# Performance work log

Measured on AMD Instinct MI355X. Metric: run time of the kernel, lower is better.

Reference implementation:

```python
import jax, jax.numpy as jnp
import numpy as np

Y0 = 0.28209479177387814  # Y_0^0 spherical harmonic (degree-0 basis)
CUTOFF = 4.6
K_COUL = 0.529
ENERGY_STD = 1.0
HEADS = 8
N, E, C, L, MID = 32768, 524288, 16, 4, 32
KC = C // 2  # channels_div = 2 -> key/value channels


def _radial(ef, W1, b1, W2, b2, W3, b3):
    # radial profile MLP producing per-edge conv weights
    h = jax.nn.relu(ef @ W1 + b1)
    h = jax.nn.relu(h @ W2 + b2)
    return h @ W3 + b3


def _conv_msg(x_src, ef, bscale, W1, b1, W2, b2, W3, b3, c_out, c_in):
    # degree-0 tensor-field conv: per-edge weight matrix times source feats, times basis
    R = _radial(ef, W1, b1, W2, b2, W3, b3).reshape(-1, c_out, c_in)
    return jnp.einsum('eoi,ei->eo', R, x_src) * bscale[:, None]


def _forward(species, src, dst, rel_pos, emb, kv_W1, kv_b1, kv_W2, kv_b2, kv_W3, kv_b3, Wq, Wproj, fin_W1, fin_b1, fin_W2, fin_b2, fin_W3, fin_b3, Wself, mlp_W1, mlp_b1, mlp_W2, mlp_b2, mlp_W3, mlp_b3):
    n = species.shape[0]
    dist = jnp.linalg.norm(rel_pos, axis=1)
    xc = dist / CUTOFF
    in_cut = dist < CUTOFF
    x2 = jnp.minimum(jnp.where(in_cut, xc * xc, 0.0), 1.0 - 1e-6)
    scale = jnp.where(in_cut, jnp.exp(3.0 - 3.0 / (1.0 - x2)), 0.0)  # bump_fn k=3
    bscale = Y0 * scale  # basis scaled by cutoff envelope per edge
    semb = emb[species - 1]          # [N,C]
    x = semb                         # degree-0 node feats
    # edge feats: (C-1) zero radial-basis channels + distance
    ef = jnp.concatenate([jnp.zeros((dist.shape[0], C - 1), dist.dtype), dist[:, None]], axis=1)
    dh = KC // HEADS
    for l in range(kv_W1.shape[0]):
        kv = _conv_msg(x[src], ef, bscale, kv_W1[l], kv_b1[l], kv_W2[l], kv_b2[l], kv_W3[l], kv_b3[l], 2 * KC, C)
        val, key_ = kv[:, :KC], kv[:, KC:]
        q = x @ Wq[l].T              # [N,KC]
        logits = jnp.einsum('ehd,ehd->eh', key_.reshape(-1, HEADS, dh), q[dst].reshape(-1, HEADS, dh)) / np.sqrt(dh)
        mx = jax.ops.segment_max(logits, dst, num_segments=n)
        w = scale[:, None] * jnp.exp(logits - mx[dst])   # weighted edge softmax
        denom = jax.ops.segment_sum(w, dst, num_segments=n)
        attn = w / jnp.maximum(denom[dst], 1e-20)
        z = (attn[:, :, None] * val.reshape(-1, HEADS, dh)).reshape(-1, KC)
        agg = jax.ops.segment_sum(z, dst, num_segments=n)
        x = jnp.concatenate([agg, x], axis=1) @ Wproj[l].T  # project(cat(attn_out, skip))
        ef = ef + x[src]             # edge feature update via copy_u
    m = _conv_msg(x[src], ef, bscale, fin_W1, fin_b1, fin_W2, fin_b2, fin_W3, fin_b3, C, C)
    feats = jax.ops.segment_sum(m, dst, num_segments=n) + x @ Wself.T  # pooled conv + self-interaction
    cat = jnp.concatenate([semb, feats], axis=1)
    h = jax.nn.silu(cat @ mlp_W1 + mlp_b1)
    h = jax.nn.silu(h @ mlp_W2 + mlp_b2)
    learned = (h @ mlp_W3 + mlp_b3)[:, 0]
    Z = species.astype(dist.dtype)
    Zu, Zv = Z[src], Z[dst]
    raw = K_COUL * Zu * Zv / (2.0 * dist)
    au = 0.8854 * 0.529 / (Zu ** 0.23 + Zv ** 0.23)
    xx = dist / au
    screen = (0.1818 * jnp.exp(-3.2 * xx) + 0.5099 * jnp.exp(-0.9423 * xx)
              + 0.2802 * jnp.exp(-0.4028 * xx) + 0.02817 * jnp.exp(-0.2016 * xx))
    coul = jax.ops.segment_sum(raw * screen * scale, dst, num_segments=n) / ENERGY_STD
    atom_e = (learned + coul) * ENERGY_STD
    return jnp.sum(atom_e)  # SumPooling over a single graph, forces=False


def setup_inputs() -> dict:
    key = jax.random.key(0)
    ks = jax.random.split(key, 32)
    species = jax.random.randint(ks[0], (N,), 1, 90, dtype=jnp.int32)
    src = jax.random.randint(ks[1], (E,), 0, N, dtype=jnp.int32)
    dst = jax.random.randint(ks[2], (E,), 0, N, dtype=jnp.int32)
    d = jax.random.normal(ks[3], (E, 3))
    d = d / jnp.linalg.norm(d, axis=1, keepdims=True)
    r = jax.random.uniform(ks[4], (E, 1), minval=0.5, maxval=5.5)
    rel_pos = (d * r).astype(jnp.float32)
    g = lambda k, sh, fan: (jax.random.normal(k, sh) / np.sqrt(fan)).astype(jnp.float32)
    return dict(
        species=species, src=src, dst=dst, rel_pos=rel_pos,
        emb=g(ks[5], (100, C), 1),
        kv_W1=g(ks[6], (L, C, MID), C), kv_b1=jnp.zeros((L, MID), jnp.float32),
        kv_W2=g(ks[7], (L, MID, MID), MID), kv_b2=jnp.zeros((L, MID), jnp.float32),
        kv_W3=g(ks[8], (L, MID, 2 * KC * C), MID), kv_b3=jnp.zeros((L, 2 * KC * C), jnp.float32),
        Wq=g(ks[9], (L, KC, C), C),
        Wproj=g(ks[10], (L, C, KC + C), KC + C),
        fin_W1=g(ks[11], (C, MID), C), fin_b1=jnp.zeros((MID,), jnp.float32),
        fin_W2=g(ks[12], (MID, MID), MID), fin_b2=jnp.zeros((MID,), jnp.float32),
        fin_W3=g(ks[13], (MID, C * C), MID), fin_b3=jnp.zeros((C * C,), jnp.float32),
        Wself=g(ks[14], (C, C), C),
        mlp_W1=g(ks[15], (2 * C, C), 2 * C), mlp_b1=jnp.zeros((C,), jnp.float32),
        mlp_W2=g(ks[16], (C, C), C), mlp_b2=jnp.zeros((C,), jnp.float32),
        mlp_W3=g(ks[17], (C, 1), C), mlp_b3=jnp.zeros((1,), jnp.float32),
    )


def reference(species, src, dst, rel_pos, emb, kv_W1, kv_b1, kv_W2, kv_b2, kv_W3, kv_b3, Wq, Wproj, fin_W1, fin_b1, fin_W2, fin_b2, fin_W3, fin_b3, Wself, mlp_W1, mlp_b1, mlp_W2, mlp_b2, mlp_W3, mlp_b3):
    return _forward(species, src, dst, rel_pos, emb, kv_W1, kv_b1, kv_W2, kv_b2, kv_W3, kv_b3, Wq, Wproj, fin_W1, fin_b1, fin_W2, fin_b2, fin_W3, fin_b3, Wself, mlp_W1, mlp_b1, mlp_W2, mlp_b2, mlp_W3, mlp_b3)
```

## Files before the change

kernel.cpp:

```cpp
#include <hip/hip_runtime.h>

constexpr float F_Y0     = 0.28209479177387814f;
constexpr float F_CUTOFF = 4.6f;

typedef short short8 __attribute__((ext_vector_type(8)));
typedef float f32x4  __attribute__((ext_vector_type(4)));
typedef float float2v __attribute__((ext_vector_type(2)));

__device__ __forceinline__ float siluf(float v) { return v / (1.0f + __expf(-v)); }

__device__ __forceinline__ unsigned pk2(float a, float b) {
  unsigned r;
  asm("v_cvt_pk_bf16_f32 %0, %1, %2" : "=v"(r) : "v"(a), "v"(b));
  return r;
}
__device__ __forceinline__ float xbf(unsigned d, int h) {
  return __uint_as_float(h ? (d & 0xffff0000u) : (d << 16));
}
__device__ __forceinline__ float2v pkmul2(float2v a, float2v b) {
  float2v d;
  asm("v_pk_mul_f32 %0, %1, %2" : "=v"(d) : "v"(a), "v"(b));
  return d;
}

union FragU { uint4 u; short8 s; };

__device__ __forceinline__ void load16(const float* p, float* r) {
  const float4* p4 = (const float4*)p;
#pragma unroll
  for (int i = 0; i < 4; i++) {
    float4 t = p4[i];
    r[4*i] = t.x; r[4*i+1] = t.y; r[4*i+2] = t.z; r[4*i+3] = t.w;
  }
}
__device__ __forceinline__ void store16(float* p, const float* r) {
  float4* p4 = (float4*)p;
#pragma unroll
  for (int i = 0; i < 4; i++) p4[i] = make_float4(r[4*i], r[4*i+1], r[4*i+2], r[4*i+3]);
}

__device__ __forceinline__ void block_reduce_store(float v, float* part) {
  __shared__ float sred[4];
  int tid = threadIdx.x;
#pragma unroll
  for (int off = 32; off > 0; off >>= 1) v += __shfl_down(v, off, 64);
  if ((tid & 63) == 0) sred[tid >> 6] = v;
  __syncthreads();
  if (tid == 0) part[blockIdx.x] = sred[0] + sred[1] + sred[2] + sred[3];
}

__global__ __launch_bounds__(256) void k_pre(
    const int* __restrict__ species, const int* __restrict__ src, const int* __restrict__ dst,
    const float* __restrict__ rel_pos,
    float* __restrict__ dist_, float* __restrict__ scale_,
    int* __restrict__ cnt,
    float* __restrict__ coul_part, int E)
{
  int e = blockIdx.x * 256 + threadIdx.x;
  float ce = 0.0f;
  if (e < E) {
    float px = rel_pos[3*(size_t)e + 0];
    float py = rel_pos[3*(size_t)e + 1];
    float pz = rel_pos[3*(size_t)e + 2];
    float dist = sqrtf(px*px + py*py + pz*pz);
    float xc = dist * (1.0f / F_CUTOFF);
    bool in_cut = dist < F_CUTOFF;
    float x2 = in_cut ? xc * xc : 0.0f;
    x2 = fminf(x2, 1.0f - 1e-6f);
    float sc = in_cut ? __expf(3.0f - 3.0f / (1.0f - x2)) : 0.0f;
    dist_[e] = dist;
    scale_[e] = sc;
    atomicAdd(&cnt[dst[e]], 1);
    float Zu = (float)species[src[e]];
    float Zv = (float)species[dst[e]];
    float raw = 0.529f * Zu * Zv / (2.0f * dist);
    float au = 0.8854f * 0.529f / (__powf(Zu, 0.23f) + __powf(Zv, 0.23f));
    float xx = dist / au;
    float screen = 0.1818f   * __expf(-3.2f    * xx)
                 + 0.5099f   * __expf(-0.9423f * xx)
                 + 0.2802f   * __expf(-0.4028f * xx)
                 + 0.02817f  * __expf(-0.2016f * xx);
    ce = raw * screen * sc;
  }
  block_reduce_store(ce, coul_part);
}

__global__ __launch_bounds__(256) void k_scan1(
    const int* __restrict__ cnt, int* __restrict__ row_ptr, int* __restrict__ bsum)
{
  __shared__ int s[256];
  int tid = threadIdx.x;
  int n = blockIdx.x * 256 + tid;
  int v = cnt[n];
  s[tid] = v;
  __syncthreads();
#pragma unroll
  for (int off = 1; off < 256; off <<= 1) {
    int t = (tid >= off) ? s[tid - off] : 0;
    __syncthreads();
    s[tid] += t;
    __syncthreads();
  }
  row_ptr[n] = s[tid] - v;
  if (tid == 255) bsum[blockIdx.x] = s[255];
}

__global__ __launch_bounds__(128) void k_scan2(int* __restrict__ bsum, int* __restrict__ boff)
{
  __shared__ int s[128];
  int tid = threadIdx.x;
  int v = bsum[tid];
  s[tid] = v;
  __syncthreads();
#pragma unroll
  for (int off = 1; off < 128; off <<= 1) {
    int t = (tid >= off) ? s[tid - off] : 0;
    __syncthreads();
    s[tid] += t;
    __syncthreads();
  }
  boff[tid] = s[tid] - v;
}

__global__ __launch_bounds__(256) void k_scan3(
    int* __restrict__ row_ptr, int* __restrict__ row_cur,
    const int* __restrict__ boff, int N, int E)
{
  int n = blockIdx.x * 256 + threadIdx.x;
  int rp = row_ptr[n] + boff[blockIdx.x];
  row_ptr[n] = rp;
  row_cur[n] = rp;
  if (n == 0) row_ptr[N] = E;
}

__global__ __launch_bounds__(256) void k_scatter_perm(
    const int* __restrict__ dst, int* __restrict__ row_cur,
    int* __restrict__ perm, int E)
{
  int e = blockIdx.x * 256 + threadIdx.x;
  if (e >= E) return;
  int pos = atomicAdd(&row_cur[dst[e]], 1);
  perm[pos] = e;
}

__global__ __launch_bounds__(256) void k_permute(
    const int* __restrict__ perm,
    const int* __restrict__ src, const float* __restrict__ dist_, const float* __restrict__ scale_,
    int* __restrict__ srcP, float* __restrict__ distP, float* __restrict__ scaleP, int E)
{
  int i = blockIdx.x * 256 + threadIdx.x;
  if (i >= E) return;
  int e = perm[i];
  srcP[i]   = src[e];
  distP[i]  = dist_[e];
  scaleP[i] = scale_[e];
}

__global__ __launch_bounds__(256) void k_prepack(
    const float* __restrict__ kv_W3, const float* __restrict__ kv_b3,
    const float* __restrict__ fin_W3, const float* __restrict__ fin_b3,
    const float* __restrict__ kv_W2, const float* __restrict__ fin_W2,
    const float* __restrict__ kv_W1, const float* __restrict__ fin_W1,
    uint4* __restrict__ WF)
{
  int t = blockIdx.x * 256 + threadIdx.x;
  if (t >= 5 * 21 * 64) return;
  int lyr = t / (21 * 64);
  int rem = t - lyr * 21 * 64;
  int f = rem >> 6;
  int l = rem & 63;
  int qq = l >> 4;
  int o = l & 15;
  const float* W3 = (lyr < 4) ? (kv_W3 + (size_t)lyr * 32 * 256) : fin_W3;
  const float* B3 = (lyr < 4) ? (kv_b3 + (size_t)lyr * 256) : fin_b3;
  const float* W2 = (lyr < 4) ? (kv_W2 + (size_t)lyr * 32 * 32) : fin_W2;
  const float* W1 = (lyr < 4) ? (kv_W1 + (size_t)lyr * 16 * 32) : fin_W1;
  float v[8];
#pragma unroll
  for (int j = 0; j < 8; j++) {
    if (f < 16) {
      int kk = f * 32 + qq * 8 + j;
      int m = kk >> 4, i = kk & 15;
      v[j] = W3[m * 256 + o * 16 + i];
    } else if (f == 16) {
      int r = qq * 8 + j;
      int mp = r >> 4, i = r & 15;
      v[j] = mp ? 0.0f : B3[o * 16 + i];
    } else if (f < 19) {
      int c = f - 17;
      int p = qq * 8 + j;
      int m = (p & 1) ? (16 + (p >> 1)) : (p >> 1);
      v[j] = W2[m * 32 + c * 16 + o];
    } else {
      int c = f - 19;
      int k = qq * 8 + j;
      v[j] = (k < 16) ? W1[k * 32 + c * 16 + o] : 0.0f;
    }
  }
  uint4 dw;
  dw.x = pk2(v[0], v[1]);
  dw.y = pk2(v[2], v[3]);
  dw.z = pk2(v[4], v[5]);
  dw.w = pk2(v[6], v[7]);
  WF[t] = dw;
}

__global__ __launch_bounds__(256) void k_node_init(
    const int* __restrict__ species, const float* __restrict__ emb,
    const float* __restrict__ Wq0,
    float* __restrict__ x, float* __restrict__ q, int N)
{
  int n = blockIdx.x * 256 + threadIdx.x;
  if (n >= N) return;
  int sp = species[n] - 1;
  float xv[16];
  load16(emb + (size_t)sp * 16, xv);
  store16(x + (size_t)n * 16, xv);
  float qv[8];
#pragma unroll
  for (int h = 0; h < 8; h++) {
    float a = 0.f;
#pragma unroll
    for (int i = 0; i < 16; i++) a += Wq0[h * 16 + i] * xv[i];
    qv[h] = a;
  }
  float4* qp = (float4*)(q + (size_t)n * 8);
  qp[0] = make_float4(qv[0], qv[1], qv[2], qv[3]);
  qp[1] = make_float4(qv[4], qv[5], qv[6], qv[7]);
}

template <int MODE>
__global__ __launch_bounds__(256, 7) void k_edge_conv(
    const int* __restrict__ srcP,
    const float* __restrict__ scaleP, const float* __restrict__ distP,
    const float* __restrict__ xsum, const float* __restrict__ x,
    const float* __restrict__ W1, const float* __restrict__ B1,
    const float* __restrict__ B2,
    const uint4* __restrict__ WF,
    unsigned* __restrict__ kvB, int E)
{
  __shared__ unsigned smem[4 * 1344];
  int tid = threadIdx.x;
  int w = __builtin_amdgcn_readfirstlane(tid >> 6);
  int l = tid & 63;
  int quad = l >> 4;
  int lo = l & 15;
  unsigned* WS  = smem + w * 1344;
  unsigned* P   = WS;
  float*    xsS = (float*)WS;
  unsigned* xsB = WS + 320;
  unsigned* efB = WS + 512;
  unsigned* h1P = WS + 704;
  unsigned* h2P = WS + 1024;

  int ebw = blockIdx.x * 64 + w * 16;

  float b2a = B2[lo], b2b = B2[16 + lo];
  float scv[4];
#pragma unroll
  for (int r = 0; r < 4; r++) scv[r] = scaleP[ebw + quad * 4 + r];

  {
    int e4 = l >> 2, c4 = l & 3;
    int s4 = srcP[ebw + e4];
    float4 xv4 = ((const float4*)(x + (size_t)s4 * 16))[c4];
    float4 ev4;
    if (MODE == 2) {
      ev4 = ((const float4*)(xsum + (size_t)s4 * 16))[c4];
      if (c4 == 3) ev4.w += distP[ebw + e4];
    }
    *(float4*)&xsS[e4 * 20 + c4 * 4] = xv4;
    uint2 xp; xp.x = pk2(xv4.x, xv4.y); xp.y = pk2(xv4.z, xv4.w);
    *(uint2*)&xsB[e4 * 12 + c4 * 2] = xp;
    if (MODE == 2) {
      uint2 ep; ep.x = pk2(ev4.x, ev4.y); ep.y = pk2(ev4.z, ev4.w);
      *(uint2*)&efB[e4 * 12 + c4 * 2] = ep;
    }
  }

  if (MODE == 0) {
    float dd = distP[ebw + lo];
#pragma unroll
    for (int jj = 0; jj < 4; jj++) {
      int d = quad * 4 + jj;
      float v0 = fmaxf(B1[d]      + dd * W1[15 * 32 + d],      0.f);
      float v1 = fmaxf(B1[d + 16] + dd * W1[15 * 32 + d + 16], 0.f);
      h1P[lo * 20 + d] = pk2(v0, v1);
    }
  } else {
    float b1a = B1[lo], b1b = B1[16 + lo];
    FragU a, b0, b1;
    uint4 r = *(const uint4*)&efB[lo * 12 + (quad & 1) * 4];
    uint4 z = make_uint4(0, 0, 0, 0);
    a.u = (quad >= 2) ? z : r;
    b0.u = WF[19 * 64 + l];
    b1.u = WF[20 * 64 + l];
    f32x4 c0 = {0.f, 0.f, 0.f, 0.f};
    f32x4 c1 = {0.f, 0.f, 0.f, 0.f};
    c0 = __builtin_amdgcn_mfma_f32_16x16x32_bf16(a.s, b0.s, c0, 0, 0, 0);
    c1 = __builtin_amdgcn_mfma_f32_16x16x32_bf16(a.s, b1.s, c1, 0, 0, 0);
#pragma unroll
    for (int r2 = 0; r2 < 4; r2++)
      h1P[(quad * 4 + r2) * 20 + lo] =
          pk2(fmaxf(c0[r2] + b1a, 0.f), fmaxf(c1[r2] + b1b, 0.f));
  }

  {
    FragU a, b0, b1;
    a.u = *(const uint4*)&h1P[lo * 20 + quad * 4];
    b0.u = WF[17 * 64 + l];
    b1.u = WF[18 * 64 + l];
    f32x4 hc0 = {0.f, 0.f, 0.f, 0.f};
    f32x4 hc1 = {0.f, 0.f, 0.f, 0.f};
    hc0 = __builtin_amdgcn_mfma_f32_16x16x32_bf16(a.s, b0.s, hc0, 0, 0, 0);
    hc1 = __builtin_amdgcn_mfma_f32_16x16x32_bf16(a.s, b1.s, hc1, 0, 0, 0);
#pragma unroll
    for (int r = 0; r < 4; r++)
      h2P[(quad * 4 + r) * 20 + lo] =
          pk2(fmaxf(hc0[r] + b2a, 0.f), fmaxf(hc1[r] + b2b, 0.f));
  }

  float2v xs2[8];
  {
    const float4* xr = (const float4*)&xsS[lo * 20];
#pragma unroll
    for (int i = 0; i < 4; i++) {
      float4 t = xr[i];
      float2v a; a.x = t.x; a.y = t.y;
      float2v b; b.x = t.z; b.y = t.w;
      xs2[2 * i]     = a;
      xs2[2 * i + 1] = b;
    }
  }
  uint2 hA = *(const uint2*)&h2P[lo * 20 + quad * 2];
  uint2 hB = *(const uint2*)&h2P[lo * 20 + 8 + quad * 2];
  float hmv[8];
  hmv[0] = xbf(hA.x, 0); hmv[1] = xbf(hA.y, 0);
  hmv[2] = xbf(hB.x, 0); hmv[3] = xbf(hB.y, 0);
  hmv[4] = xbf(hA.x, 1); hmv[5] = xbf(hA.y, 1);
  hmv[6] = xbf(hB.x, 1); hmv[7] = xbf(hB.y, 1);

  f32x4 acc = {0.f, 0.f, 0.f, 0.f};
  {
    FragU a, b;
    uint4 r = *(const uint4*)&xsB[lo * 12 + (quad & 1) * 4];
    uint4 z = make_uint4(0, 0, 0, 0);
    a.u = (quad >= 2) ? z : r;
    b.u = WF[16 * 64 + l];
    acc = __builtin_amdgcn_mfma_f32_16x16x32_bf16(a.s, b.s, acc, 0, 0, 0);
  }

#pragma unroll
  for (int q = 0; q < 4; q++) {
#pragma unroll
    for (int j = 0; j < 2; j++) {
      float hm = hmv[q * 2 + j];
      float2v hm2; hm2.x = hm; hm2.y = hm;
      uint4 d0, d1;
      float2v p0 = pkmul2(hm2, xs2[0]);
      float2v p1 = pkmul2(hm2, xs2[1]);
      float2v p2 = pkmul2(hm2, xs2[2]);
      float2v p3 = pkmul2(hm2, xs2[3]);
      d0.x = pk2(p0.x, p0.y); d0.y = pk2(p1.x, p1.y);
      d0.z = pk2(p2.x, p2.y); d0.w = pk2(p3.x, p3.y);
      float2v p4 = pkmul2(hm2, xs2[4]);
      float2v p5 = pkmul2(hm2, xs2[5]);
      float2v p6 = pkmul2(hm2, xs2[6]);
      float2v p7 = pkmul2(hm2, xs2[7]);
      d1.x = pk2(p4.x, p4.y); d1.y = pk2(p5.x, p5.y);
      d1.z = pk2(p6.x, p6.y); d1.w = pk2(p7.x, p7.y);
      int cb = quad * 4 + j * 2;
      *(uint4*)&P[lo * 64 + (((cb)     ^ lo) << 2)] = d0;
      *(uint4*)&P[lo * 64 + (((cb + 1) ^ lo) << 2)] = d1;
    }
#pragma unroll
    for (int t = 0; t < 4; t++) {
      FragU a, b;
      a.u = *(const uint4*)&P[lo * 64 + (((t * 4 + quad) ^ lo) << 2)];
      b.u = WF[(q * 4 + t) * 64 + l];
      acc = __builtin_amdgcn_mfma_f32_16x16x32_bf16(a.s, b.s, acc, 0, 0, 0);
    }
  }

#pragma unroll
  for (int r = 0; r < 4; r++) {
    int e = quad * 4 + r;
    ((float*)h2P)[e * 20 + lo] = acc[r] * (F_Y0 * scv[r]);
  }
  {
    int e2 = l >> 2, c = l & 3;
    const float* row = (const float*)&h2P[e2 * 20 + c * 4];
    float4 t = *(const float4*)row;
    uint2 pkd;
    pkd.x = pk2(t.x, t.y);
    pkd.y = pk2(t.z, t.w);
    *(uint2*)(kvB + ((size_t)(ebw + e2) * 8 + c * 2)) = pkd;
  }
}

template <bool INIT>
__global__ __launch_bounds__(256) void k_agg_update(
    const int* __restrict__ row_ptr, const float* __restrict__ scaleP,
    const unsigned* __restrict__ kvB, const float* __restrict__ qin,
    const float* __restrict__ xin,
    const float* __restrict__ Wproj, const float* __restrict__ Wq_next,
    float* __restrict__ xout, float* __restrict__ qout, float* __restrict__ xsum, int N)
{
  __shared__ float sA[16 * 8];
  __shared__ float sX[16 * 17];
  __shared__ float sN[16 * 17];
  int tid = threadIdx.x;
  int nl = tid >> 4;
  int t16 = tid & 15;
  int h = t16 & 7;
  int p = t16 >> 3;
  int n = blockIdx.x * 16 + nl;
  int hd = h >> 1, hh = h & 1;

  float qh = qin[(size_t)n * 8 + h];
  int j0 = row_ptr[n], j1 = row_ptr[n + 1];
  float num = 0.f, den = 0.f;
  for (int j = j0 + p; j < j1; j += 2) {
    float val = xbf(kvB[(size_t)j * 8 + hd], hh);
    float key = xbf(kvB[(size_t)j * 8 + 4 + hd], hh);
    float lg = fminf(key * qh, 60.0f);
    float wv = scaleP[j] * __expf(lg);
    num += wv * val;
    den += wv;
  }
  num += __shfl_xor(num, 8, 64);
  den += __shfl_xor(den, 8, 64);
  if (p == 0) sA[nl * 8 + h] = num / fmaxf(den, 1e-20f);
  sX[nl * 17 + t16] = xin[(size_t)n * 16 + t16];
  __syncthreads();

  float cat[24];
#pragma unroll
  for (int j = 0; j < 8; j++) cat[j] = sA[nl * 8 + j];
#pragma unroll
  for (int j = 0; j < 16; j++) cat[8 + j] = sX[nl * 17 + j];
  float xn = 0.f;
#pragma unroll
  for (int j = 0; j < 24; j++) xn += Wproj[t16 * 24 + j] * cat[j];
  xout[(size_t)n * 16 + t16] = xn;
  if (INIT) {
    xsum[(size_t)n * 16 + t16] = xn;
  } else {
    xsum[(size_t)n * 16 + t16] += xn;
  }
  sN[nl * 17 + t16] = xn;
  __syncthreads();

  if (p == 0) {
    float a = 0.f;
#pragma unroll
    for (int i = 0; i < 16; i++) a += Wq_next[h * 16 + i] * sN[nl * 17 + i];
    qout[(size_t)n * 8 + h] = a;
  }
}

__global__ __launch_bounds__(256) void k_feats_final(
    const int* __restrict__ row_ptr, const unsigned* __restrict__ kvB,
    const float* __restrict__ x,
    const int* __restrict__ species, const float* __restrict__ emb,
    const float* __restrict__ Wself,
    const float* __restrict__ mW1, const float* __restrict__ mb1,
    const float* __restrict__ mW2, const float* __restrict__ mb2,
    const float* __restrict__ mW3, const float* __restrict__ mb3,
    float* __restrict__ learn_part, int N)
{
  __shared__ float sX[16 * 20];
  __shared__ float sC[16 * 40];
  __shared__ float sH[16 * 20];
  int tid = threadIdx.x;
  int nl = tid >> 4;
  int o = tid & 15;
  int n = blockIdx.x * 16 + nl;
  int od = o >> 1, oh = o & 1;

  int j0 = row_ptr[n], j1 = row_ptr[n + 1];
  float ft = 0.f;
  for (int j = j0; j < j1; ++j) ft += xbf(kvB[(size_t)j * 8 + od], oh);

  if (o < 4) {
    float4 v = ((const float4*)(x + (size_t)n * 16))[o];
    *(float4*)&sX[nl * 20 + o * 4] = v;
  } else if (o < 8) {
    int sp = species[n] - 1;
    float4 v = ((const float4*)(emb + (size_t)sp * 16))[o - 4];
    *(float4*)&sC[nl * 40 + (o - 4) * 4] = v;
  }
  __syncthreads();

  float xv[16];
  load16(&sX[nl * 20], xv);
  float a = ft;
#pragma unroll
  for (int i = 0; i < 16; i++) a += Wself[o * 16 + i] * xv[i];
  sC[nl * 40 + 16 + o] = a;
  __syncthreads();

  float cat[32];
  load16(&sC[nl * 40], cat);
  load16(&sC[nl * 40 + 16], cat + 16);
  float hh = mb1[o];
#pragma unroll
  for (int k = 0; k < 32; k++) hh += cat[k] * mW1[k * 16 + o];
  hh = siluf(hh);
  sH[nl * 20 + o] = hh;
  __syncthreads();

  float hv[16];
  load16(&sH[nl * 20], hv);
  float h2 = mb2[o];
#pragma unroll
  for (int k = 0; k < 16; k++) h2 += hv[k] * mW2[k * 16 + o];
  h2 = siluf(h2);
  float contrib = h2 * mW3[o] + ((o == 0) ? mb3[0] : 0.f);
  block_reduce_store(contrib, learn_part);
}

__global__ __launch_bounds__(256) void k_finalize(
    const float* __restrict__ coul_part, int nc,
    const float* __restrict__ learn_part, int nl,
    float* __restrict__ out)
{
  __shared__ float sred[4];
  int tid = threadIdx.x;
  float v = 0.f;
  for (int i = tid; i < nc; i += 256) v += coul_part[i];
  for (int i = tid; i < nl; i += 256) v += learn_part[i];
#pragma unroll
  for (int off = 32; off > 0; off >>= 1) v += __shfl_down(v, off, 64);
  if ((tid & 63) == 0) sred[tid >> 6] = v;
  __syncthreads();
  if (tid == 0) out[0] = sred[0] + sred[1] + sred[2] + sred[3];
}

extern "C" void kernel_launch(void* const* d_in, const int* in_sizes, int n_in,
                              void* d_out, int out_size, void* d_ws, size_t ws_size,
                              hipStream_t stream)
{
  const int*   species = (const int*)d_in[0];
  const int*   src     = (const int*)d_in[1];
  const int*   dst     = (const int*)d_in[2];
  const float* rel_pos = (const float*)d_in[3];
  const float* emb     = (const float*)d_in[4];
  const float* kv_W1   = (const float*)d_in[5];
  const float* kv_b1   = (const float*)d_in[6];
  const float* kv_W2   = (const float*)d_in[7];
  const float* kv_b2   = (const float*)d_in[8];
  const float* kv_W3   = (const float*)d_in[9];
  const float* kv_b3   = (const float*)d_in[10];
  const float* Wq      = (const float*)d_in[11];
  const float* Wproj   = (const float*)d_in[12];
  const float* fin_W1  = (const float*)d_in[13];
  const float* fin_b1  = (const float*)d_in[14];
  const float* fin_W2  = (const float*)d_in[15];
  const float* fin_b2  = (const float*)d_in[16];
  const float* fin_W3  = (const float*)d_in[17];
  const float* fin_b3  = (const float*)d_in[18];
  const float* Wself   = (const float*)d_in[19];
  const float* mlp_W1  = (const float*)d_in[20];
  const float* mlp_b1  = (const float*)d_in[21];
  const float* mlp_W2  = (const float*)d_in[22];
  const float* mlp_b2  = (const float*)d_in[23];
  const float* mlp_W3  = (const float*)d_in[24];
  const float* mlp_b3  = (const float*)d_in[25];

  const int N = in_sizes[0];
  const int E = in_sizes[1];
  const int nblk_e = (E + 255) / 256;
  const int nblk_n = (N + 255) / 256;
  const int nblk_f = N / 16;

  char* p = (char*)d_ws;
  auto alloc = [&](size_t bytes) -> void* {
    void* r = (void*)p;
    p += (bytes + 255) & ~(size_t)255;
    return r;
  };
  float*    dist_   = (float*)alloc((size_t)E * 4);
  float*    scale_  = (float*)alloc((size_t)E * 4);
  float*    distP   = (float*)alloc((size_t)E * 4);
  float*    scaleP  = (float*)alloc((size_t)E * 4);
  int*      srcP    = (int*)  alloc((size_t)E * 4);
  int*      perm    = (int*)  alloc((size_t)E * 4);
  unsigned* kvB     = (unsigned*)alloc((size_t)E * 8 * 4);
  float*    xA      = (float*)alloc((size_t)N * 16 * 4);
  float*    xB      = (float*)alloc((size_t)N * 16 * 4);
  float*    xsum    = (float*)alloc((size_t)N * 16 * 4);
  float*    q       = (float*)alloc((size_t)N * 8 * 4);
  int*      cnt     = (int*)  alloc((size_t)N * 4);
  int*      row_ptr = (int*)  alloc((size_t)(N + 1) * 4);
  int*      row_cur = (int*)  alloc((size_t)N * 4);
  int*      bsum    = (int*)  alloc(128 * 4);
  int*      boff    = (int*)  alloc(128 * 4);
  uint4*    WF      = (uint4*)alloc((size_t)5 * 21 * 64 * 16);
  float*    coul_part  = (float*)alloc((size_t)nblk_e * 4);
  float*    learn_part = (float*)alloc((size_t)nblk_f * 4);

  dim3 blk(256);
  dim3 egrid(nblk_e);
  dim3 cgrid(E / 64);
  dim3 ngrid(nblk_n);
  dim3 augrid(N / 16);
  dim3 fgrid(nblk_f);

  hipMemsetAsync(cnt, 0, (size_t)N * 4, stream);

  k_prepack<<<dim3(27), blk, 0, stream>>>(kv_W3, kv_b3, fin_W3, fin_b3,
                                          kv_W2, fin_W2, kv_W1, fin_W1, WF);

  k_pre<<<egrid, blk, 0, stream>>>(species, src, dst, rel_pos, dist_, scale_,
                                   cnt, coul_part, E);
  k_scan1<<<ngrid, blk, 0, stream>>>(cnt, row_ptr, bsum);
  k_scan2<<<dim3(1), dim3(128), 0, stream>>>(bsum, boff);
  k_scan3<<<ngrid, blk, 0, stream>>>(row_ptr, row_cur, boff, N, E);
  k_scatter_perm<<<egrid, blk, 0, stream>>>(dst, row_cur, perm, E);
  k_permute<<<egrid, blk, 0, stream>>>(perm, src, dist_, scale_,
                                       srcP, distP, scaleP, E);

  k_node_init<<<ngrid, blk, 0, stream>>>(species, emb, Wq, xA, q, N);

  float* xin = xA;
  float* xout = xB;
  for (int l = 0; l < 4; l++) {
    const float* W1 = kv_W1 + (size_t)l * 16 * 32;
    const float* B1 = kv_b1 + (size_t)l * 32;
    const float* B2 = kv_b2 + (size_t)l * 32;
    const uint4* WFl = WF + (size_t)l * 21 * 64;
    const float* Wqn = Wq + (size_t)((l < 3) ? (l + 1) : 0) * 8 * 16;
    if (l == 0) {
      k_edge_conv<0><<<cgrid, blk, 0, stream>>>(srcP, scaleP, distP, xsum, xin,
                                                W1, B1, B2, WFl, kvB, E);
    } else {
      k_edge_conv<2><<<cgrid, blk, 0, stream>>>(srcP, scaleP, distP, xsum, xin,
                                                W1, B1, B2, WFl, kvB, E);
    }
    if (l == 0) {
      k_agg_update<true><<<augrid, blk, 0, stream>>>(row_ptr, scaleP, kvB, q, xin,
                                                     Wproj, Wqn, xout, q, xsum, N);
    } else {
      k_agg_update<false><<<augrid, blk, 0, stream>>>(row_ptr, scaleP, kvB, q, xin,
                                                      Wproj + (size_t)l * 16 * 24, Wqn,
                                                      xout, q, xsum, N);
    }
    float* tmp = xin; xin = xout; xout = tmp;
  }

  k_edge_conv<2><<<cgrid, blk, 0, stream>>>(srcP, scaleP, distP, xsum, xin,
                                            fin_W1, fin_b1, fin_b2,
                                            WF + (size_t)4 * 21 * 64, kvB, E);
  k_feats_final<<<fgrid, blk, 0, stream>>>(row_ptr, kvB, xin, species, emb, Wself,
                                           mlp_W1, mlp_b1, mlp_W2, mlp_b2, mlp_W3, mlp_b3,
                                           learn_part, N);
  k_finalize<<<dim3(1), blk, 0, stream>>>(coul_part, nblk_e, learn_part, nblk_f,
                                          (float*)d_out);
}
```

Baseline: 419.3 us.

## Fuse edge permutation into scatter and use wave-per-node aggregation

Merges the perm-scatter and gather-permute kernels so edge attributes are written directly to their CSR slot, removing the perm array and one pass over the edges. The node aggregation and final feature kernels are remapped from 16 threads per node to one 64-lane wave per node. Edges are split across 8 or 4 lane groups and combined with xor shuffles, and block barriers are dropped in favour of intra-wave LDS communication. This raises parallelism over edge lists at the cost of more idle lanes in the small per-node matmuls, and it relies on wave lockstep for LDS visibility.

```diff
diff --git a/kernel.cpp b/kernel.cpp
--- a/kernel.cpp
+++ b/kernel.cpp
@@ -134,26 +134,17 @@
 }
 
 __global__ __launch_bounds__(256) void k_scatter_perm(
-    const int* __restrict__ dst, int* __restrict__ row_cur,
-    int* __restrict__ perm, int E)
+    const int* __restrict__ src, const int* __restrict__ dst,
+    const float* __restrict__ dist_, const float* __restrict__ scale_,
+    int* __restrict__ row_cur,
+    int* __restrict__ srcP, float* __restrict__ distP, float* __restrict__ scaleP, int E)
 {
   int e = blockIdx.x * 256 + threadIdx.x;
   if (e >= E) return;
   int pos = atomicAdd(&row_cur[dst[e]], 1);
-  perm[pos] = e;
-}
-
-__global__ __launch_bounds__(256) void k_permute(
-    const int* __restrict__ perm,
-    const int* __restrict__ src, const float* __restrict__ dist_, const float* __restrict__ scale_,
-    int* __restrict__ srcP, float* __restrict__ distP, float* __restrict__ scaleP, int E)
-{
-  int i = blockIdx.x * 256 + threadIdx.x;
-  if (i >= E) return;
-  int e = perm[i];
-  srcP[i]   = src[e];
-  distP[i]  = dist_[e];
-  scaleP[i] = scale_[e];
+  srcP[pos]   = src[e];
+  distP[pos]  = dist_[e];
+  scaleP[pos] = scale_[e];
 }
 
 __global__ __launch_bounds__(256) void k_prepack(
@@ -406,21 +397,24 @@
     const float* __restrict__ Wproj, const float* __restrict__ Wq_next,
     float* __restrict__ xout, float* __restrict__ qout, float* __restrict__ xsum, int N)
 {
-  __shared__ float sA[16 * 8];
-  __shared__ float sX[16 * 17];
-  __shared__ float sN[16 * 17];
+  __shared__ float sA[4 * 8];
+  __shared__ float sX[4 * 16];
+  __shared__ float sN[4 * 16];
   int tid = threadIdx.x;
-  int nl = tid >> 4;
-  int t16 = tid & 15;
-  int h = t16 & 7;
-  int p = t16 >> 3;
-  int n = blockIdx.x * 16 + nl;
+  int w = __builtin_amdgcn_readfirstlane(tid >> 6);
+  int l = tid & 63;
+  int h = l & 7;
+  int s = l >> 3;
+  int t16 = l & 15;
+  int n = blockIdx.x * 4 + w;
   int hd = h >> 1, hh = h & 1;
+
+  if (l < 16) sX[w * 16 + t16] = xin[(size_t)n * 16 + t16];
 
   float qh = qin[(size_t)n * 8 + h];
   int j0 = row_ptr[n], j1 = row_ptr[n + 1];
   float num = 0.f, den = 0.f;
-  for (int j = j0 + p; j < j1; j += 2) {
+  for (int j = j0 + s; j < j1; j += 8) {
     float val = xbf(kvB[(size_t)j * 8 + hd], hh);
     float key = xbf(kvB[(size_t)j * 8 + 4 + hd], hh);
     float lg = fminf(key * qh, 60.0f);
@@ -428,33 +422,32 @@
     num += wv * val;
     den += wv;
   }
-  num += __shfl_xor(num, 8, 64);
-  den += __shfl_xor(den, 8, 64);
-  if (p == 0) sA[nl * 8 + h] = num / fmaxf(den, 1e-20f);
-  sX[nl * 17 + t16] = xin[(size_t)n * 16 + t16];
-  __syncthreads();
-
-  float cat[24];
-#pragma unroll
-  for (int j = 0; j < 8; j++) cat[j] = sA[nl * 8 + j];
-#pragma unroll
-  for (int j = 0; j < 16; j++) cat[8 + j] = sX[nl * 17 + j];
-  float xn = 0.f;
-#pragma unroll
-  for (int j = 0; j < 24; j++) xn += Wproj[t16 * 24 + j] * cat[j];
-  xout[(size_t)n * 16 + t16] = xn;
-  if (INIT) {
-    xsum[(size_t)n * 16 + t16] = xn;
-  } else {
-    xsum[(size_t)n * 16 + t16] += xn;
-  }
-  sN[nl * 17 + t16] = xn;
-  __syncthreads();
-
-  if (p == 0) {
+  num += __shfl_xor(num, 8, 64);  den += __shfl_xor(den, 8, 64);
+  num += __shfl_xor(num, 16, 64); den += __shfl_xor(den, 16, 64);
+  num += __shfl_xor(num, 32, 64); den += __shfl_xor(den, 32, 64);
+  if (l < 8) sA[w * 8 + h] = num / fmaxf(den, 1e-20f);
+
+  if (l < 16) {
+    float cat[24];
+#pragma unroll
+    for (int j = 0; j < 8; j++) cat[j] = sA[w * 8 + j];
+#pragma unroll
+    for (int j = 0; j < 16; j++) cat[8 + j] = sX[w * 16 + j];
+    float xn = 0.f;
+#pragma unroll
+    for (int j = 0; j < 24; j++) xn += Wproj[t16 * 24 + j] * cat[j];
+    xout[(size_t)n * 16 + t16] = xn;
+    if (INIT) {
+      xsum[(size_t)n * 16 + t16] = xn;
+    } else {
+      xsum[(size_t)n * 16 + t16] += xn;
+    }
+    sN[w * 16 + t16] = xn;
+  }
+  if (l < 8) {
     float a = 0.f;
 #pragma unroll
-    for (int i = 0; i < 16; i++) a += Wq_next[h * 16 + i] * sN[nl * 17 + i];
+    for (int i = 0; i < 16; i++) a += Wq_next[h * 16 + i] * sN[w * 16 + i];
     qout[(size_t)n * 8 + h] = a;
   }
 }
@@ -469,54 +462,58 @@
     const float* __restrict__ mW3, const float* __restrict__ mb3,
     float* __restrict__ learn_part, int N)
 {
-  __shared__ float sX[16 * 20];
-  __shared__ float sC[16 * 40];
-  __shared__ float sH[16 * 20];
+  __shared__ float sX[4 * 16];
+  __shared__ float sC[4 * 32];
+  __shared__ float sH[4 * 16];
   int tid = threadIdx.x;
-  int nl = tid >> 4;
-  int o = tid & 15;
-  int n = blockIdx.x * 16 + nl;
+  int w = __builtin_amdgcn_readfirstlane(tid >> 6);
+  int l = tid & 63;
+  int o = l & 15;
+  int s = l >> 4;
+  int n = blockIdx.x * 4 + w;
   int od = o >> 1, oh = o & 1;
+
+  if (l < 4) {
+    float4 v = ((const float4*)(x + (size_t)n * 16))[l];
+    *(float4*)&sX[w * 16 + l * 4] = v;
+  } else if (l < 8) {
+    int sp = species[n] - 1;
+    float4 v = ((const float4*)(emb + (size_t)sp * 16))[l - 4];
+    *(float4*)&sC[w * 32 + (l - 4) * 4] = v;
+  }
 
   int j0 = row_ptr[n], j1 = row_ptr[n + 1];
   float ft = 0.f;
-  for (int j = j0; j < j1; ++j) ft += xbf(kvB[(size_t)j * 8 + od], oh);
-
-  if (o < 4) {
-    float4 v = ((const float4*)(x + (size_t)n * 16))[o];
-    *(float4*)&sX[nl * 20 + o * 4] = v;
-  } else if (o < 8) {
-    int sp = species[n] - 1;
-    float4 v = ((const float4*)(emb + (size_t)sp * 16))[o - 4];
-    *(float4*)&sC[nl * 40 + (o - 4) * 4] = v;
-  }
-  __syncthreads();
-
-  float xv[16];
-  load16(&sX[nl * 20], xv);
-  float a = ft;
-#pragma unroll
-  for (int i = 0; i < 16; i++) a += Wself[o * 16 + i] * xv[i];
-  sC[nl * 40 + 16 + o] = a;
-  __syncthreads();
-
-  float cat[32];
-  load16(&sC[nl * 40], cat);
-  load16(&sC[nl * 40 + 16], cat + 16);
-  float hh = mb1[o];
-#pragma unroll
-  for (int k = 0; k < 32; k++) hh += cat[k] * mW1[k * 16 + o];
-  hh = siluf(hh);
-  sH[nl * 20 + o] = hh;
-  __syncthreads();
-
-  float hv[16];
-  load16(&sH[nl * 20], hv);
-  float h2 = mb2[o];
-#pragma unroll
-  for (int k = 0; k < 16; k++) h2 += hv[k] * mW2[k * 16 + o];
-  h2 = siluf(h2);
-  float contrib = h2 * mW3[o] + ((o == 0) ? mb3[0] : 0.f);
+  for (int j = j0 + s; j < j1; j += 4) ft += xbf(kvB[(size_t)j * 8 + od], oh);
+  ft += __shfl_xor(ft, 16, 64);
+  ft += __shfl_xor(ft, 32, 64);
+
+  float contrib = 0.f;
+  if (l < 16) {
+    float xv[16];
+    load16(&sX[w * 16], xv);
+    float a = ft;
+#pragma unroll
+    for (int i = 0; i < 16; i++) a += Wself[o * 16 + i] * xv[i];
+    sC[w * 32 + 16 + o] = a;
+
+    float cat[32];
+    load16(&sC[w * 32], cat);
+    load16(&sC[w * 32 + 16], cat + 16);
+    float h1v = mb1[o];
+#pragma unroll
+    for (int k = 0; k < 32; k++) h1v += cat[k] * mW1[k * 16 + o];
+    h1v = siluf(h1v);
+    sH[w * 16 + o] = h1v;
+
+    float hv[16];
+    load16(&sH[w * 16], hv);
+    float h2v = mb2[o];
+#pragma unroll
+    for (int k = 0; k < 16; k++) h2v += hv[k] * mW2[k * 16 + o];
+    h2v = siluf(h2v);
+    contrib = h2v * mW3[o] + ((o == 0) ? mb3[0] : 0.f);
+  }
   block_reduce_store(contrib, learn_part);
 }
 
@@ -572,7 +569,7 @@
   const int E = in_sizes[1];
   const int nblk_e = (E + 255) / 256;
   const int nblk_n = (N + 255) / 256;
-  const int nblk_f = N / 16;
+  const int nblk_f = N / 4;
 
   char* p = (char*)d_ws;
   auto alloc = [&](size_t bytes) -> void* {
@@ -585,7 +582,6 @@
   float*    distP   = (float*)alloc((size_t)E * 4);
   float*    scaleP  = (float*)alloc((size_t)E * 4);
   int*      srcP    = (int*)  alloc((size_t)E * 4);
-  int*      perm    = (int*)  alloc((size_t)E * 4);
   unsigned* kvB     = (unsigned*)alloc((size_t)E * 8 * 4);
   float*    xA      = (float*)alloc((size_t)N * 16 * 4);
   float*    xB      = (float*)alloc((size_t)N * 16 * 4);
@@ -604,7 +600,7 @@
   dim3 egrid(nblk_e);
   dim3 cgrid(E / 64);
   dim3 ngrid(nblk_n);
-  dim3 augrid(N / 16);
+  dim3 augrid(N / 4);
   dim3 fgrid(nblk_f);
 
   hipMemsetAsync(cnt, 0, (size_t)N * 4, stream);
@@ -617,9 +613,8 @@
   k_scan1<<<ngrid, blk, 0, stream>>>(cnt, row_ptr, bsum);
   k_scan2<<<dim3(1), dim3(128), 0, stream>>>(bsum, boff);
   k_scan3<<<ngrid, blk, 0, stream>>>(row_ptr, row_cur, boff, N, E);
-  k_scatter_perm<<<egrid, blk, 0, stream>>>(dst, row_cur, perm, E);
-  k_permute<<<egrid, blk, 0, stream>>>(perm, src, dist_, scale_,
-                                       srcP, distP, scaleP, E);
+  k_scatter_perm<<<egrid, blk, 0, stream>>>(src, dst, dist_, scale_, row_cur,
+                                            srcP, distP, scaleP, E);
 
   k_node_init<<<ngrid, blk, 0, stream>>>(species, emb, Wq, xA, q, N);
 
```

After: 457.7 us. +9.2%, slower.
